# Kernel tuning notes

Hardware: AMD Instinct MI355X
Metric: run time of the kernel (lower is better)

Reference implementation:

```python
import jax, jax.numpy as jnp
import numpy as np

EPS = 1.0 / 137.0
NUM_HEADS = 16


def yat_dense(x, kernel, bias, alpha):
    y = jnp.einsum('btc,cf->btf', x, kernel)
    x2 = jnp.sum(x * x, axis=-1, keepdims=True)          # [B,T,1]
    k2 = jnp.sum(kernel * kernel, axis=0)                 # [F]
    y = (y * y) / (x2 + k2 - 2.0 * y + EPS)
    out_f = kernel.shape[1]
    scale = (jnp.sqrt(jnp.float32(out_f)) / jnp.log1p(jnp.float32(out_f))) ** alpha
    return y * scale + bias


def setup_inputs() -> dict:
    key = jax.random.key(0)
    ks = jax.random.split(key, 6)
    B, T, C = 2, 1024, 1024
    x = jax.random.normal(ks[0], (B, T, C), dtype=jnp.float32)
    mask = jnp.tril(jnp.ones((T, T), dtype=bool))[None, None, :, :]  # causal [1,1,T,T]
    w_qkv = jax.random.normal(ks[1], (C, 3 * C), dtype=jnp.float32) * 0.02
    b_qkv = jnp.zeros((3 * C,), dtype=jnp.float32)
    alpha_qkv = jnp.ones((1,), dtype=jnp.float32)
    w_proj = jax.random.normal(ks[2], (C, C), dtype=jnp.float32) * 0.02
    b_proj = jnp.zeros((C,), dtype=jnp.float32)
    alpha_proj = jnp.ones((1,), dtype=jnp.float32)
    alpha_attn = jnp.ones((1,), dtype=jnp.float32)
    return {"x": x, "mask": mask, "w_qkv": w_qkv, "b_qkv": b_qkv,
            "alpha_qkv": alpha_qkv, "w_proj": w_proj, "b_proj": b_proj,
            "alpha_proj": alpha_proj, "alpha_attn": alpha_attn}


def reference(x, mask, w_qkv, b_qkv, alpha_qkv, w_proj, b_proj, alpha_proj, alpha_attn):
    B, T, C = x.shape
    head_dim = C // NUM_HEADS
    scale = jnp.log1p(jnp.float32(head_dim))
    inv_scale = (head_dim / scale) ** alpha_attn  # [1]

    qkv = yat_dense(x, w_qkv, b_qkv, alpha_qkv)               # [B,T,3C]
    qkv = qkv.reshape(B, T, 3, NUM_HEADS, head_dim)
    q, k, v = jnp.moveaxis(qkv, 2, 0)                         # each [B,T,H,hd]
    # NOTE: source transposes with (0,3,1,2) -> [B, head_dim, T, H]; reproduced faithfully.
    q = jnp.transpose(q, (0, 3, 1, 2))
    k = jnp.transpose(k, (0, 3, 1, 2))
    v = jnp.transpose(v, (0, 3, 1, 2))

    dot = jnp.einsum('bhid,bhjd->bhij', q, k)                 # [B,hd,T,T]
    sq_dot = dot * dot
    q2 = jnp.sum(q * q, axis=-1, keepdims=True)               # [B,hd,T,1]
    k2 = jnp.sum(k * k, axis=-1, keepdims=True).transpose(0, 1, 3, 2)  # [B,hd,1,T]
    sq_dist = q2 + k2 - 2.0 * dot
    attn = sq_dot / (sq_dist + EPS)
    attn = attn * inv_scale
    attn = jnp.where(mask, attn, jnp.finfo(jnp.float32).min)
    attn = jax.nn.softmax(attn, axis=-1)

    out = jnp.einsum('bhij,bhjd->bhid', attn, v)              # [B,hd,T,H]
    out = out.transpose(0, 2, 1, 3).reshape(B, T, C)
    out = yat_dense(out, w_proj, b_proj, alpha_proj)
    return out
```

## Files before the change

### kernel.cpp

```cpp
#include <hip/hip_runtime.h>
#include <math.h>

#define YAT_EPS (1.0f / 137.0f)


typedef __bf16 bf16x8 __attribute__((ext_vector_type(8)));
typedef float floatx4 __attribute__((ext_vector_type(4)));
typedef unsigned int uintx4 __attribute__((ext_vector_type(4)));

__device__ __forceinline__ float fast_rcp(float x) {
#if __has_builtin(__builtin_amdgcn_rcpf)
    return __builtin_amdgcn_rcpf(x);
#else
    return 1.0f / x;
#endif
}
__device__ __forceinline__ float fast_exp2(float x) {
#if __has_builtin(__builtin_amdgcn_exp2f)
    return __builtin_amdgcn_exp2f(x);
#else
    return exp2f(x);
#endif
}

__device__ __forceinline__ unsigned short f32_bf16(float f) {
    unsigned u = __builtin_bit_cast(unsigned, f);
    u += 0x7fffu + ((u >> 16) & 1u);
    return (unsigned short)(u >> 16);
}
__device__ __forceinline__ float bf16_f32(unsigned short h) {
    unsigned u = ((unsigned)h) << 16;
    return __builtin_bit_cast(float, u);
}

__global__ __launch_bounds__(256) void prep_kernel(
    const float* __restrict__ x,
    const float* __restrict__ w_qkv, const float* __restrict__ w_proj,
    unsigned short* __restrict__ xh, unsigned short* __restrict__ xl,
    float* __restrict__ x2x,
    unsigned short* __restrict__ WtQh, unsigned short* __restrict__ WtQl,
    float* __restrict__ k2q,
    unsigned short* __restrict__ WtPh, unsigned short* __restrict__ WtPl,
    float* __restrict__ k2p)
{
    __shared__ float t[32][33];
    const int bid = blockIdx.x;
    const int tid = threadIdx.x;

    if (bid < 4096) {
        const bool isQ = bid < 3072;
        const float* W = isQ ? w_qkv : w_proj;
        unsigned short* th = isQ ? WtQh : WtPh;
        unsigned short* tl = isQ ? WtQl : WtPl;
        float* k2 = isQ ? k2q : k2p;
        const int N = isQ ? 3072 : 1024;
        const int id2 = isQ ? bid : bid - 3072;
        const int nx = isQ ? (id2 % 96) : (id2 & 31);
        const int ky = isQ ? (id2 / 96) : (id2 >> 5);
        const int tx = tid & 31, ty = tid >> 5;
        const int n0 = nx * 32, k0 = ky * 32;
        #pragma unroll
        for (int r = 0; r < 4; ++r)
            t[ty + r * 8][tx] = W[(size_t)(k0 + ty + r * 8) * N + n0 + tx];
        __syncthreads();
        #pragma unroll
        for (int r = 0; r < 4; ++r) {
            const int nl = ty + r * 8;
            const int nn = n0 + nl;
            int nw = nn;
            if (isQ) {
                nw = (nn & ~1023) | (((nn & 63) >> 3) << 7)
                   | (((nn >> 6) & 15) << 3) | (nn & 7);
            }
            const float v = t[tx][nl];
            const unsigned short h = f32_bf16(v);
            th[(size_t)nw * 1024 + k0 + tx] = h;
            tl[(size_t)nw * 1024 + k0 + tx] = f32_bf16(v - bf16_f32(h));
            float s = v * v;
            #pragma unroll
            for (int m = 16; m > 0; m >>= 1) s += __shfl_xor(s, m, 32);
            if (tx == 0) atomicAdd(&k2[nn], s);
        }
    } else {
        const int row = bid - 4096;
        float* red = &t[0][0];
        float4 v = *(const float4*)(x + (size_t)row * 1024 + tid * 4);
        float vv[4] = {v.x, v.y, v.z, v.w};
        unsigned short hh[4], ll[4];
        float s = 0.0f;
        #pragma unroll
        for (int e = 0; e < 4; ++e) {
            hh[e] = f32_bf16(vv[e]);
            ll[e] = f32_bf16(vv[e] - bf16_f32(hh[e]));
            s = fmaf(vv[e], vv[e], s);
        }
        *(ushort4*)(xh + (size_t)row * 1024 + tid * 4) =
            make_ushort4(hh[0], hh[1], hh[2], hh[3]);
        *(ushort4*)(xl + (size_t)row * 1024 + tid * 4) =
            make_ushort4(ll[0], ll[1], ll[2], ll[3]);
        #pragma unroll
        for (int off = 32; off > 0; off >>= 1) s += __shfl_down(s, off, 64);
        if ((tid & 63) == 0) red[tid >> 6] = s;
        __syncthreads();
        if (tid == 0) x2x[row] = red[0] + red[1] + red[2] + red[3];
    }
}

template <int BM, int BN, int BK, int MODE, int MINW>
__global__ __launch_bounds__(256, MINW) void gemm_yat_mfma_kernel(
    const unsigned short* __restrict__ Ah, const unsigned short* __restrict__ Al,
    const unsigned short* __restrict__ Bh, const unsigned short* __restrict__ Bl,
    const float* __restrict__ bias, const float* __restrict__ x2,
    const float* __restrict__ k2, const float* __restrict__ alphap,
    float* __restrict__ out, int N, int K, float scale_base,
    unsigned short* __restrict__ kvu, float* __restrict__ q2k,
    float* __restrict__ k2k)
{
    constexpr int TM = (BM / 2) / 16;
    constexpr int TN = (BN / 2) / 16;
    constexpr int ASZ = BM * BK;
    constexpr int BSZ = BN * BK;
    constexpr int AB  = ASZ * 2;
    constexpr int BB  = BSZ * 2;
    constexpr int NI  = (BM + BN) * BK / 1024;
    constexpr int LPR = BK / 8;
    __shared__ __align__(16) unsigned short sbuf[2 * (ASZ + BSZ)];

    const int tid = threadIdx.x;
    const int w = tid >> 6, l = tid & 63;
    const int lane16 = l & 15, quad = l >> 4;
    const int wm = w & 1, wn = w >> 1;
    const int m0 = blockIdx.y * BM, n0 = blockIdx.x * BN;

    floatx4 acc[TM][TN];
    #pragma unroll
    for (int tm = 0; tm < TM; ++tm)
        #pragma unroll
        for (int tn = 0; tn < TN; ++tn)
            acc[tm][tn] = (floatx4){0.f, 0.f, 0.f, 0.f};

    for (int k0 = 0; k0 < K; k0 += BK) {
        __syncthreads();
        #pragma unroll
        for (int i = 0; i < NI; ++i) {
            const int o = (i * 4 + w) * 1024;
            const unsigned short* gp;
            if (o < 2 * AB) {
                const unsigned short* g = (o < AB) ? Ah : Al;
                const int oo = o & (AB - 1);
                gp = g + (size_t)(m0 + oo / (BK * 2) + l / LPR) * K
                       + k0 + (l % LPR) * 8;
            } else {
                const int ob = o - 2 * AB;
                const unsigned short* g = (ob < BB) ? Bh : Bl;
                const int oo = ob & (BB - 1);
                gp = g + (size_t)(n0 + oo / (BK * 2) + l / LPR) * K
                       + k0 + (l % LPR) * 8;
            }
            __builtin_amdgcn_global_load_lds(
                (const __attribute__((address_space(1))) unsigned int*)gp,
                (__attribute__((address_space(3))) unsigned int*)((char*)sbuf + o),
                16, 0, 0);
        }
        __syncthreads();

        #pragma unroll
        for (int kk = 0; kk < BK / 32; ++kk) {
            bf16x8 afh[TM], afl[TM], bfh[TN], bfl[TN];
            #pragma unroll
            for (int tm = 0; tm < TM; ++tm) {
                const int base = (wm * (BM / 2) + tm * 16 + lane16) * BK
                               + kk * 32 + quad * 8;
                afh[tm] = *(const bf16x8*)(sbuf + base);
                afl[tm] = *(const bf16x8*)(sbuf + ASZ + base);
            }
            #pragma unroll
            for (int tn = 0; tn < TN; ++tn) {
                const int nb = (wn * (BN / 2) + tn * 16 + lane16) * BK
                             + kk * 32 + quad * 8;
                bfh[tn] = *(const bf16x8*)(sbuf + 2 * ASZ + nb);
                bfl[tn] = *(const bf16x8*)(sbuf + 2 * ASZ + BSZ + nb);
            }
            #pragma unroll
            for (int tm = 0; tm < TM; ++tm)
                #pragma unroll
                for (int tn = 0; tn < TN; ++tn) {
                    acc[tm][tn] = __builtin_amdgcn_mfma_f32_16x16x32_bf16(
                        afh[tm], bfh[tn], acc[tm][tn], 0, 0, 0);
                    acc[tm][tn] = __builtin_amdgcn_mfma_f32_16x16x32_bf16(
                        afh[tm], bfl[tn], acc[tm][tn], 0, 0, 0);
                    acc[tm][tn] = __builtin_amdgcn_mfma_f32_16x16x32_bf16(
                        afl[tm], bfh[tn], acc[tm][tn], 0, 0, 0);
                }
        }
    }

    const float scale = powf(scale_base, alphap[0]);

    if (MODE == 0) {
        #pragma unroll
        for (int tm = 0; tm < TM; ++tm) {
            #pragma unroll
            for (int tn = 0; tn < TN; ++tn) {
                const int n = n0 + wn * (BN / 2) + tn * 16 + lane16;
                const float kk = k2[n];
                const float bb = bias[n];
                const int mrow = m0 + wm * (BM / 2) + tm * 16 + quad * 4;
                #pragma unroll
                for (int r = 0; r < 4; ++r) {
                    const float y = acc[tm][tn][r];
                    const float den = x2[mrow + r] + kk - 2.0f * y + YAT_EPS;
                    out[(size_t)(mrow + r) * N + n] =
                        y * y / den * scale + bb;
                }
            }
        }
    } else {
        constexpr int G = BM / 32;
        float* lds = (float*)sbuf;
        const int s_ = n0 >> 10;
        const int dblk = (n0 >> 7) & 7;
        const int b_ = m0 >> 10;
        const int tl = tid >> 3;
        const int ddr = tid & 7;
        const int d_glob = dblk * 8 + ddr;

        #pragma unroll
        for (int g = 0; g < G; ++g) {
            __syncthreads();
            if constexpr (G == 1) {
                #pragma unroll
                for (int tn = 0; tn < TN; ++tn) {
                    const int n = n0 + wn * (BN / 2) + tn * 16 + lane16;
                    const int hcol = (n >> 3) & 15;
                    const int norig = (n & ~1023) | (hcol << 6)
                                    | (dblk << 3) | (n & 7);
                    const float kk = k2[norig];
                    const float bb = bias[norig];
                    const int mrow = m0 + wm * 16 + quad * 4;
                    const int tbase = wm * 16 + quad * 4;
                    const int col = wn * (BN / 2) + tn * 16 + lane16;
                    #pragma unroll
                    for (int r = 0; r < 4; ++r) {
                        const float y = acc[0][tn][r];
                        const float den =
                            x2[mrow + r] + kk - 2.0f * y + YAT_EPS;
                        lds[(tbase + r) * 132 + col] =
                            y * y / den * scale + bb;
                    }
                }
            } else {
                constexpr int GH = (G > 1) ? (G / 2) : 1;
                if (wm == g / GH) {
                    const int gl = g % GH;
                    #pragma unroll
                    for (int tm2 = 0; tm2 < 2; ++tm2) {
                        const int tm = gl * 2 + tm2;
                        #pragma unroll
                        for (int tn = 0; tn < TN; ++tn) {
                            const int n = n0 + wn * (BN / 2) + tn * 16 + lane16;
                            const int hcol = (n >> 3) & 15;
                            const int norig = (n & ~1023) | (hcol << 6)
                                            | (dblk << 3) | (n & 7);
                            const float kk = k2[norig];
                            const float bb = bias[norig];
                            const int mrow =
                                m0 + wm * (BM / 2) + tm * 16 + quad * 4;
                            const int tbase = tm2 * 16 + quad * 4;
                            const int col = wn * (BN / 2) + tn * 16 + lane16;
                            #pragma unroll
                            for (int r = 0; r < 4; ++r) {
                                const float y = acc[tm][tn][r];
                                const float den =
                                    x2[mrow + r] + kk - 2.0f * y + YAT_EPS;
                                lds[(tbase + r) * 132 + col] =
                                    y * y / den * scale + bb;
                            }
                        }
                    }
                }
            }
            __syncthreads();

            float y[16];
            #pragma unroll
            for (int h = 0; h < 16; ++h)
                y[h] = lds[tl * 132 + h * 8 + ddr];
            const int t_glob = (m0 & 1023) + g * 32 + tl;

            if (s_ < 2) {
                unsigned short hb[16], lb[16];
                float s2 = 0.f;
                #pragma unroll
                for (int h = 0; h < 16; ++h) {
                    hb[h] = f32_bf16(y[h]);
                    lb[h] = f32_bf16(y[h] - bf16_f32(hb[h]));
                    s2 = fmaf(y[h], y[h], s2);
                }
                unsigned short* dst = kvu + (size_t)b_ * 6291456
                    + (s_ == 0 ? 4194304u : 0u)
                    + ((size_t)(d_glob * 1024 + t_glob)) * 32;
                #pragma unroll
                for (int h4 = 0; h4 < 4; ++h4) {
                    *(ushort4*)(dst + h4 * 4) = make_ushort4(
                        hb[h4*4], hb[h4*4+1], hb[h4*4+2], hb[h4*4+3]);
                    *(ushort4*)(dst + 16 + h4 * 4) = make_ushort4(
                        lb[h4*4], lb[h4*4+1], lb[h4*4+2], lb[h4*4+3]);
                }
                float* sq = (s_ == 0) ? q2k : k2k;
                sq[b_ * 65536 + d_glob * 1024 + t_glob] = s2;
            } else {
                const int j = t_glob;
                const int jt2 = j >> 5;
                const int e = ((j >> 4) & 1) * 4 + (j & 3);
                const int qd = (j >> 2) & 3;
                unsigned short* dst = kvu + (size_t)b_ * 6291456 + 2097152
                    + d_glob * 32768 + jt2 * 1024 + qd * 128 + e;
                #pragma unroll
                for (int h = 0; h < 16; ++h) {
                    const unsigned short vh = f32_bf16(y[h]);
                    dst[h * 8] = vh;
                    dst[512 + h * 8] = f32_bf16(y[h] - bf16_f32(vh));
                }
            }
        }
    }
}

__global__ __launch_bounds__(256, 4) void yat_attn_mfma2_kernel(
    const unsigned short* __restrict__ KVU,
    const float* __restrict__ k2k, const float* __restrict__ q2k,
    const float* __restrict__ alphap,
    unsigned short* __restrict__ attn_h, unsigned short* __restrict__ attn_l,
    float* __restrict__ x2a)
{
    const int tid = threadIdx.x;
    const int lane = tid & 63, w = tid >> 6;
    const int lane16 = lane & 15, quad = lane >> 4;
    const int d = blockIdx.x, c = blockIdx.y, b = blockIdx.z;

    const float isc =
        powf(64.0f / log1pf(64.0f), alphap[0]) * 1.44269504f;

    const unsigned short* kp = KVU + (size_t)b * 6291456 + d * 32768;
    const unsigned short* vp = KVU + (size_t)b * 6291456 + 2097152 + d * 32768;
    const unsigned short* qp = KVU + (size_t)b * 6291456 + 4194304 + d * 32768;
    const float* k2bd = k2k + b * 65536 + d * 1024;
    const float* q2bd = q2k + b * 65536 + d * 1024;

    const int ti0 = c * 4 + w;
    const int tiA = ti0, tiB = 63 - ti0;

    const bf16x8 qA = *(const bf16x8*)(qp + (tiA * 16 + lane16) * 32 + quad * 8);
    const bf16x8 qB = *(const bf16x8*)(qp + (tiB * 16 + lane16) * 32 + quad * 8);
    const float q2A = q2bd[tiA * 16 + lane16] + YAT_EPS;
    const float q2B = q2bd[tiB * 16 + lane16] + YAT_EPS;
    const int iA = tiA * 16 + lane16;
    const int iB = tiB * 16 + lane16;

    floatx4 OA = (floatx4){0.f, 0.f, 0.f, 0.f};
    floatx4 OB = (floatx4){0.f, 0.f, 0.f, 0.f};
    float lsA = 0.f, lsB = 0.f;

    const int lastA = tiA >> 1, lastB = tiB >> 1;

    for (int jt2 = 0; jt2 <= lastB; ++jt2) {
        const int j0 = jt2 * 32;
        const unsigned short* kp0 = kp + (j0 + lane16) * 32;
        const unsigned short* kp1 = kp + (j0 + 16 + lane16) * 32;
        const bf16x8 k0a = *(const bf16x8*)(kp0 + quad * 8);
        const bf16x8 k0b = *(const bf16x8*)(kp0 + ((quad ^ 2) * 8));
        const bf16x8 k1a = *(const bf16x8*)(kp1 + quad * 8);
        const bf16x8 k1b = *(const bf16x8*)(kp1 + ((quad ^ 2) * 8));
        const unsigned short* vpj = vp + jt2 * 1024 + quad * 128 + lane16 * 8;
        const bf16x8 vh = *(const bf16x8*)(vpj);
        const bf16x8 vl = *(const bf16x8*)(vpj + 512);
        const float4 k20 = *(const float4*)(k2bd + j0 + quad * 4);
        const float4 k21 = *(const float4*)(k2bd + j0 + 16 + quad * 4);
        const float k2r[8] = {k20.x, k20.y, k20.z, k20.w,
                              k21.x, k21.y, k21.z, k21.w};
        const int jbase0 = j0 + quad * 4;

        #pragma unroll
        for (int half = 0; half < 2; ++half) {
            if (half == 0 && jt2 > lastA) continue;
            const bf16x8 qf = half ? qB : qA;
            const float q2e = half ? q2B : q2A;
            const int iM = half ? iB : iA;
            floatx4 S0 = __builtin_amdgcn_mfma_f32_16x16x32_bf16(
                k0a, qf, (floatx4){0.f, 0.f, 0.f, 0.f}, 0, 0, 0);
            S0 = __builtin_amdgcn_mfma_f32_16x16x32_bf16(k0b, qf, S0, 0, 0, 0);
            floatx4 S1 = __builtin_amdgcn_mfma_f32_16x16x32_bf16(
                k1a, qf, (floatx4){0.f, 0.f, 0.f, 0.f}, 0, 0, 0);
            S1 = __builtin_amdgcn_mfma_f32_16x16x32_bf16(k1b, qf, S1, 0, 0, 0);

            float p[8], lsum = 0.f;
            #pragma unroll
            for (int e = 0; e < 8; ++e) {
                const float s = (e < 4) ? S0[e & 3] : S1[e & 3];
                const int j = jbase0 + (e >> 2) * 16 + (e & 3);
                const float den = fmaf(-2.f, s, q2e + k2r[e]);
                float pe = fast_exp2(s * s * fast_rcp(den) * isc);
                pe = (j <= iM) ? pe : 0.f;
                lsum += pe;
                p[e] = pe;
            }
            if (half) lsB += lsum; else lsA += lsum;

            unsigned ph32[4], pl32[4];
            #pragma unroll
            for (int e2 = 0; e2 < 4; ++e2) {
                const unsigned b0 = __builtin_bit_cast(unsigned, p[e2 * 2]);
                const unsigned b1 = __builtin_bit_cast(unsigned, p[e2 * 2 + 1]);
                ph32[e2] = (b0 >> 16) | (b1 & 0xFFFF0000u);
                const float f0 = p[e2 * 2] -
                    __builtin_bit_cast(float, b0 & 0xFFFF0000u);
                const float f1 = p[e2 * 2 + 1] -
                    __builtin_bit_cast(float, b1 & 0xFFFF0000u);
                pl32[e2] = (__builtin_bit_cast(unsigned, f0) >> 16) |
                           (__builtin_bit_cast(unsigned, f1) & 0xFFFF0000u);
            }
            const bf16x8 Ph = __builtin_bit_cast(bf16x8,
                (uintx4){ph32[0], ph32[1], ph32[2], ph32[3]});
            const bf16x8 Pl = __builtin_bit_cast(bf16x8,
                (uintx4){pl32[0], pl32[1], pl32[2], pl32[3]});

            floatx4 O = half ? OB : OA;
            O = __builtin_amdgcn_mfma_f32_16x16x32_bf16(Ph, vh, O, 0, 0, 0);
            O = __builtin_amdgcn_mfma_f32_16x16x32_bf16(Pl, vh, O, 0, 0, 0);
            O = __builtin_amdgcn_mfma_f32_16x16x32_bf16(Ph, vl, O, 0, 0, 0);
            if (half) OB = O; else OA = O;
        }
    }

    #pragma unroll
    for (int half = 0; half < 2; ++half) {
        float ls = half ? lsB : lsA;
        const floatx4 O = half ? OB : OA;
        const int ti = half ? tiB : tiA;
        ls += __shfl_xor(ls, 16, 64);
        ls += __shfl_xor(ls, 32, 64);
        const float linv = 1.0f / ls;
        #pragma unroll
        for (int r = 0; r < 4; ++r) {
            const float lr = __shfl(linv, quad * 4 + r, 16);
            const float v = O[r] * lr;
            const int i = ti * 16 + quad * 4 + r;
            const size_t off =
                ((size_t)(b * 1024 + i)) * 1024 + d * 16 + lane16;
            const unsigned short vh16 = f32_bf16(v);
            attn_h[off] = vh16;
            attn_l[off] = f32_bf16(v - bf16_f32(vh16));
            float s2 = v * v;
            s2 += __shfl_xor(s2, 1, 64);
            s2 += __shfl_xor(s2, 2, 64);
            s2 += __shfl_xor(s2, 4, 64);
            s2 += __shfl_xor(s2, 8, 64);
            if (lane16 == 0) atomicAdd(&x2a[b * 1024 + i], s2);
        }
    }
}

extern "C" void kernel_launch(void* const* d_in, const int* in_sizes, int n_in,
                              void* d_out, int out_size, void* d_ws, size_t ws_size,
                              hipStream_t stream)
{
    const float* x          = (const float*)d_in[0];
    const float* w_qkv      = (const float*)d_in[2];
    const float* b_qkv      = (const float*)d_in[3];
    const float* alpha_qkv  = (const float*)d_in[4];
    const float* w_proj     = (const float*)d_in[5];
    const float* b_proj     = (const float*)d_in[6];
    const float* alpha_proj = (const float*)d_in[7];
    const float* alpha_attn = (const float*)d_in[8];
    float* out = (float*)d_out;

    float* ws = (float*)d_ws;
    unsigned short* KVU  = (unsigned short*)ws;
    unsigned short* WtQh = (unsigned short*)(ws + 6291456);
    unsigned short* WtQl = (unsigned short*)(ws + 7864320);
    unsigned short* WtPh = (unsigned short*)(ws + 9437184);
    unsigned short* WtPl = (unsigned short*)(ws + 9961472);
    unsigned short* xh   = (unsigned short*)(ws + 10485760);
    unsigned short* xl   = (unsigned short*)(ws + 11534336);
    float* x2x  = ws + 12582912;
    float* x2a  = ws + 12584960;
    float* k2q  = ws + 12587008;
    float* k2p  = ws + 12590080;
    float* k2k  = ws + 12591104;
    float* q2k  = ws + 12722176;
    unsigned short* attn_h = WtQh;
    unsigned short* attn_l = WtQl;

    hipMemsetAsync(x2a, 0, (2048 + 3072 + 1024) * sizeof(float), stream);

    prep_kernel<<<6144, 256, 0, stream>>>(
        x, w_qkv, w_proj, xh, xl, x2x, WtQh, WtQl, k2q, WtPh, WtPl, k2p);

    const float sb_qkv = sqrtf(3072.0f) / log1pf(3072.0f);
    gemm_yat_mfma_kernel<64, 128, 64, 2, 3><<<dim3(24, 32), 256, 0, stream>>>(
        xh, xl, WtQh, WtQl, b_qkv, x2x, k2q, alpha_qkv, nullptr,
        3072, 1024, sb_qkv, KVU, q2k, k2k);

    yat_attn_mfma2_kernel<<<dim3(64, 8, 2), 256, 0, stream>>>(
        KVU, k2k, q2k, alpha_attn, attn_h, attn_l, x2a);

    const float sb_proj = sqrtf(1024.0f) / log1pf(1024.0f);
    gemm_yat_mfma_kernel<64, 64, 64, 0, 2><<<dim3(16, 32), 256, 0, stream>>>(
        attn_h, attn_l, WtPh, WtPl, b_proj, x2a, k2p, alpha_proj, out,
        1024, 1024, sb_proj, nullptr, nullptr, nullptr);
}
```

Measured before the change: 227.3 us.

## Vectorize weight transpose stores, skip causal masking on full tiles, add MFMA priority

The weight transpose in prep now has each thread write two bf16 values at once with ushort2 stores and reduce over 16 lanes. The zeroing of x2a moves into the prep kernel, so the memset shrinks. In attention, tiles that lie fully below the causal diagonal skip the per-element mask compare, the hi/lo packing uses v_perm, and the MFMA blocks are wrapped in s_setprio to favour matrix issue. These are several small unrelated tweaks that together cut instruction count and global-store transactions; the masking shortcut relies on the tile bound check being correct.

```diff
diff --git a/kernel.cpp b/kernel.cpp
--- a/kernel.cpp
+++ b/kernel.cpp
@@ -41,7 +41,8 @@
     unsigned short* __restrict__ WtQh, unsigned short* __restrict__ WtQl,
     float* __restrict__ k2q,
     unsigned short* __restrict__ WtPh, unsigned short* __restrict__ WtPl,
-    float* __restrict__ k2p)
+    float* __restrict__ k2p,
+    float* __restrict__ x2a)
 {
     __shared__ float t[32][33];
     const int bid = blockIdx.x;
@@ -63,23 +64,29 @@
         for (int r = 0; r < 4; ++r)
             t[ty + r * 8][tx] = W[(size_t)(k0 + ty + r * 8) * N + n0 + tx];
         __syncthreads();
-        #pragma unroll
-        for (int r = 0; r < 4; ++r) {
-            const int nl = ty + r * 8;
+        const int tx2 = tid & 15, ty2 = tid >> 4;
+        #pragma unroll
+        for (int r = 0; r < 2; ++r) {
+            const int nl = ty2 + r * 16;
             const int nn = n0 + nl;
             int nw = nn;
             if (isQ) {
                 nw = (nn & ~1023) | (((nn & 63) >> 3) << 7)
                    | (((nn >> 6) & 15) << 3) | (nn & 7);
             }
-            const float v = t[tx][nl];
-            const unsigned short h = f32_bf16(v);
-            th[(size_t)nw * 1024 + k0 + tx] = h;
-            tl[(size_t)nw * 1024 + k0 + tx] = f32_bf16(v - bf16_f32(h));
-            float s = v * v;
-            #pragma unroll
-            for (int m = 16; m > 0; m >>= 1) s += __shfl_xor(s, m, 32);
-            if (tx == 0) atomicAdd(&k2[nn], s);
+            const float v0 = t[2 * tx2][nl];
+            const float v1 = t[2 * tx2 + 1][nl];
+            const unsigned short h0 = f32_bf16(v0);
+            const unsigned short h1 = f32_bf16(v1);
+            *(ushort2*)(th + (size_t)nw * 1024 + k0 + 2 * tx2) =
+                make_ushort2(h0, h1);
+            *(ushort2*)(tl + (size_t)nw * 1024 + k0 + 2 * tx2) =
+                make_ushort2(f32_bf16(v0 - bf16_f32(h0)),
+                             f32_bf16(v1 - bf16_f32(h1)));
+            float s = fmaf(v0, v0, v1 * v1);
+            #pragma unroll
+            for (int m = 8; m > 0; m >>= 1) s += __shfl_xor(s, m, 16);
+            if (tx2 == 0) atomicAdd(&k2[nn], s);
         }
     } else {
         const int row = bid - 4096;
@@ -102,7 +109,10 @@
         for (int off = 32; off > 0; off >>= 1) s += __shfl_down(s, off, 64);
         if ((tid & 63) == 0) red[tid >> 6] = s;
         __syncthreads();
-        if (tid == 0) x2x[row] = red[0] + red[1] + red[2] + red[3];
+        if (tid == 0) {
+            x2x[row] = red[0] + red[1] + red[2] + red[3];
+            x2a[row] = 0.0f;
+        }
     }
 }
 
@@ -387,23 +397,38 @@
             const bf16x8 qf = half ? qB : qA;
             const float q2e = half ? q2B : q2A;
             const int iM = half ? iB : iA;
+            const int tiH = half ? tiB : tiA;
+
+            __builtin_amdgcn_s_setprio(1);
             floatx4 S0 = __builtin_amdgcn_mfma_f32_16x16x32_bf16(
                 k0a, qf, (floatx4){0.f, 0.f, 0.f, 0.f}, 0, 0, 0);
             S0 = __builtin_amdgcn_mfma_f32_16x16x32_bf16(k0b, qf, S0, 0, 0, 0);
             floatx4 S1 = __builtin_amdgcn_mfma_f32_16x16x32_bf16(
                 k1a, qf, (floatx4){0.f, 0.f, 0.f, 0.f}, 0, 0, 0);
             S1 = __builtin_amdgcn_mfma_f32_16x16x32_bf16(k1b, qf, S1, 0, 0, 0);
+            __builtin_amdgcn_s_setprio(0);
 
             float p[8], lsum = 0.f;
-            #pragma unroll
-            for (int e = 0; e < 8; ++e) {
-                const float s = (e < 4) ? S0[e & 3] : S1[e & 3];
-                const int j = jbase0 + (e >> 2) * 16 + (e & 3);
-                const float den = fmaf(-2.f, s, q2e + k2r[e]);
-                float pe = fast_exp2(s * s * fast_rcp(den) * isc);
-                pe = (j <= iM) ? pe : 0.f;
-                lsum += pe;
-                p[e] = pe;
+            if (j0 + 31 <= tiH * 16) {
+                #pragma unroll
+                for (int e = 0; e < 8; ++e) {
+                    const float s = (e < 4) ? S0[e & 3] : S1[e & 3];
+                    const float den = fmaf(-2.f, s, q2e + k2r[e]);
+                    const float pe = fast_exp2(s * s * fast_rcp(den) * isc);
+                    lsum += pe;
+                    p[e] = pe;
+                }
+            } else {
+                #pragma unroll
+                for (int e = 0; e < 8; ++e) {
+                    const float s = (e < 4) ? S0[e & 3] : S1[e & 3];
+                    const int j = jbase0 + (e >> 2) * 16 + (e & 3);
+                    const float den = fmaf(-2.f, s, q2e + k2r[e]);
+                    float pe = fast_exp2(s * s * fast_rcp(den) * isc);
+                    pe = (j <= iM) ? pe : 0.f;
+                    lsum += pe;
+                    p[e] = pe;
+                }
             }
             if (half) lsB += lsum; else lsA += lsum;
 
@@ -412,13 +437,14 @@
             for (int e2 = 0; e2 < 4; ++e2) {
                 const unsigned b0 = __builtin_bit_cast(unsigned, p[e2 * 2]);
                 const unsigned b1 = __builtin_bit_cast(unsigned, p[e2 * 2 + 1]);
-                ph32[e2] = (b0 >> 16) | (b1 & 0xFFFF0000u);
+                ph32[e2] = __builtin_amdgcn_perm(b1, b0, 0x07060302u);
                 const float f0 = p[e2 * 2] -
                     __builtin_bit_cast(float, b0 & 0xFFFF0000u);
                 const float f1 = p[e2 * 2 + 1] -
                     __builtin_bit_cast(float, b1 & 0xFFFF0000u);
-                pl32[e2] = (__builtin_bit_cast(unsigned, f0) >> 16) |
-                           (__builtin_bit_cast(unsigned, f1) & 0xFFFF0000u);
+                pl32[e2] = __builtin_amdgcn_perm(
+                    __builtin_bit_cast(unsigned, f1),
+                    __builtin_bit_cast(unsigned, f0), 0x07060302u);
             }
             const bf16x8 Ph = __builtin_bit_cast(bf16x8,
                 (uintx4){ph32[0], ph32[1], ph32[2], ph32[3]});
@@ -426,9 +452,11 @@
                 (uintx4){pl32[0], pl32[1], pl32[2], pl32[3]});
 
             floatx4 O = half ? OB : OA;
+            __builtin_amdgcn_s_setprio(1);
             O = __builtin_amdgcn_mfma_f32_16x16x32_bf16(Ph, vh, O, 0, 0, 0);
             O = __builtin_amdgcn_mfma_f32_16x16x32_bf16(Pl, vh, O, 0, 0, 0);
             O = __builtin_amdgcn_mfma_f32_16x16x32_bf16(Ph, vl, O, 0, 0, 0);
+            __builtin_amdgcn_s_setprio(0);
             if (half) OB = O; else OA = O;
         }
     }
@@ -492,10 +520,10 @@
     unsigned short* attn_h = WtQh;
     unsigned short* attn_l = WtQl;
 
-    hipMemsetAsync(x2a, 0, (2048 + 3072 + 1024) * sizeof(float), stream);
+    hipMemsetAsync(k2q, 0, (3072 + 1024) * sizeof(float), stream);
 
     prep_kernel<<<6144, 256, 0, stream>>>(
-        x, w_qkv, w_proj, xh, xl, x2x, WtQh, WtQl, k2q, WtPh, WtPl, k2p);
+        x, w_qkv, w_proj, xh, xl, x2x, WtQh, WtQl, k2q, WtPh, WtPl, k2p, x2a);
 
     const float sb_qkv = sqrtf(3072.0f) / log1pf(3072.0f);
     gemm_yat_mfma_kernel<64, 128, 64, 2, 3><<<dim3(24, 32), 256, 0, stream>>>(
```

Measured after the change: 219.9 us. 3.2% less time.
